# Kernel optimization log

Hardware: AMD Instinct MI355X
Metric: run time of the kernel (lower is better)

## Reference

```python
import jax, jax.numpy as jnp
import numpy as np

IN_DIM = 1024
OUT_DIM = 2048
GRID = 5   # kan_config.grid_size
K = 3      # kan_config.spline_order


def b_splines(x, grid, k):
    """Cox-de Boor recursion.
    x: (N, D), grid: (D, G+2k+1) extended knots. Returns (N, D, G+k) basis values."""
    x = x[..., None]              # (N, D, 1)
    g = grid[None, :, :]          # (1, D, M)
    # degree-0 indicator bases
    B = ((x >= g[..., :-1]) & (x < g[..., 1:])).astype(x.dtype)  # (N, D, M-1)
    for p in range(1, k + 1):
        left = (x - g[..., : -(p + 1)]) / (g[..., p:-1] - g[..., : -(p + 1)])
        right = (g[..., p + 1:] - x) / (g[..., p + 1:] - g[..., 1:-p])
        B = left * B[..., :-1] + right * B[..., 1:]
    return B  # (N, D, G+k)


def setup_inputs() -> dict:
    key = jax.random.key(0)
    k1, k2, k3 = jax.random.split(key, 3)
    # inputs kept inside the spline grid range [-1, 1]
    x = jax.random.uniform(k1, (4, 2048, IN_DIM), jnp.float32, -1.0, 1.0)
    # uniform extended grid over [-1, 1] with k extra knots on each side
    h = 2.0 / GRID
    g = jnp.arange(-K, GRID + K + 1, dtype=jnp.float32) * h - 1.0  # (G+2K+1,)
    grid = jnp.broadcast_to(g, (IN_DIM, GRID + 2 * K + 1)).astype(jnp.float32)
    coef = (jax.random.normal(k2, (IN_DIM, OUT_DIM, GRID + K), jnp.float32) * 0.1)
    scale_base = jax.random.normal(k3, (IN_DIM, OUT_DIM), jnp.float32) * 0.1 + (1.0 / np.sqrt(IN_DIM)).astype(np.float32)
    scale_sp = jnp.ones((IN_DIM, OUT_DIM), jnp.float32)
    return {"x": x, "grid": grid, "coef": coef, "scale_base": scale_base, "scale_sp": scale_sp}


def reference(x, grid, coef, scale_base, scale_sp):
    shp = x.shape
    xf = x.reshape(-1, shp[-1])                 # (N, D)
    B = b_splines(xf, grid, K)                  # (N, D, G+K)
    coef_s = coef * scale_sp[:, :, None]        # fold per-edge spline scale into coefficients
    spline = jnp.einsum('ndg,dog->no', B, coef_s)          # (N, O)
    base = jnp.einsum('nd,do->no', jax.nn.silu(xf), scale_base)  # (N, O)
    out = base + spline
    return out.reshape(shp[:-1] + (OUT_DIM,))
```

## Files before the change

### kernel.cpp

```cpp
#include <hip/hip_runtime.h>
#include <hip/hip_bf16.h>
#include <cstdint>

typedef unsigned short u16;
typedef __bf16 bf16x8 __attribute__((ext_vector_type(8)));
typedef float  f32x4  __attribute__((ext_vector_type(4)));

typedef const __attribute__((address_space(1))) void* gptr_t;
typedef __attribute__((address_space(3))) void*       sptr_t;

#define IN_DIM  1024
#define OUT_DIM 2048
#define NROWS   8192
#define NB      8
#define KTOT    (IN_DIM * 9)
#define KSPL    (IN_DIM * 8)

#define WT_O 16
#define WT_D 64
#define TR_BLOCKS ((NROWS / 64) * (IN_DIM / 64))
#define WT_BLOCKS ((OUT_DIM / WT_O) * (IN_DIM / WT_D))
#define ACT_BLOCKS ((NROWS / 64) * (IN_DIM / 64))

#define BK 32
#define TILE_U16 (256 * BK)
#define NKT (KTOT / BK)

__device__ __forceinline__ float rcp_fast(float v) { return __builtin_amdgcn_rcpf(v); }

__device__ __forceinline__ u16 f2b(float v) {
  uint32_t u = __float_as_uint(v);
  uint32_t r = (u + 0x7FFFu + ((u >> 16) & 1u)) >> 16;
  return (u16)r;
}

__device__ __forceinline__ uint32_t pkbf(float a, float b) {
  return (uint32_t)f2b(a) | ((uint32_t)f2b(b) << 16);
}

__device__ __forceinline__ uint4 basis_pack(float xval) {
  float tt = (xval + 1.0f) * 2.5f;
  float jf = floorf(tt);
  jf = fminf(fmaxf(jf, 0.0f), 4.0f);
  const float u = tt - jf;
  const int j = (int)jf;
  const float um = 1.0f - u;
  const float u2 = u * u, u3 = u2 * u;
  const float b0 = um * um * um * (1.0f / 6.0f);
  const float b1 = (3.0f * u3 - 6.0f * u2 + 4.0f) * (1.0f / 6.0f);
  const float b2 = (-3.0f * u3 + 3.0f * u2 + 3.0f * u + 1.0f) * (1.0f / 6.0f);
  const float b3 = u3 * (1.0f / 6.0f);
  const uint32_t e01 = pkbf(b0, b1), e23 = pkbf(b2, b3);
  const uint32_t o0 = e01 << 16;
  const uint32_t o12 = (e01 >> 16) | (e23 << 16);
  const uint32_t o3 = e23 >> 16;
  const int odd = j & 1, m = j >> 1;
  const uint32_t a0 = odd ? o0 : e01;
  const uint32_t a1 = odd ? o12 : e23;
  const uint32_t a2 = odd ? o3 : 0u;
  uint4 wv;
  wv.x = (m == 0) ? a0 : 0u;
  wv.y = (m == 1) ? a0 : ((m == 0) ? a1 : 0u);
  wv.z = (m == 2) ? a0 : ((m == 1) ? a1 : ((m == 0) ? a2 : 0u));
  wv.w = (m == 2) ? a1 : ((m == 1) ? a2 : 0u);
  return wv;
}

__global__ __launch_bounds__(256) void kan_prep2(const float* __restrict__ x,
                                                 const float* __restrict__ coef,
                                                 const float* __restrict__ scale_base,
                                                 const float* __restrict__ scale_sp,
                                                 u16* __restrict__ act,
                                                 u16* __restrict__ wt) {
  const int t = threadIdx.x;

  if (blockIdx.x < ACT_BLOCKS) {
    __shared__ __align__(16) u16 st[64][72];
    const int bi = blockIdx.x;
    const int n0 = (bi & 127) * 64;
    const int d0 = (bi >> 7) * 64;
    const int dl = t & 63, r0 = t >> 6;
#pragma unroll
    for (int i = 0; i < 16; ++i) {
      const int r = r0 + i * 4;
      const float v = x[(size_t)(n0 + r) * IN_DIM + d0 + dl];
      *(uint4*)&act[(size_t)(n0 + r) * KTOT + (size_t)(d0 + dl) * 8] = basis_pack(v);
      st[r][dl] = f2b(v * rcp_fast(1.0f + __expf(-v)));
    }
    __syncthreads();
#pragma unroll
    for (int j = 0; j < 2; ++j) {
      const int idx = t + j * 256;
      const int r = idx >> 3, c8 = idx & 7;
      *(uint4*)&act[(size_t)(n0 + r) * KTOT + KSPL + d0 + c8 * 8] =
          *(const uint4*)&st[r][c8 * 8];
    }
  } else {
    __shared__ __align__(16) u16 tsp[WT_O][WT_D * 8 + 8];
    __shared__ __align__(16) u16 tsi[WT_O][WT_D + 8];
    const int bi = blockIdx.x - ACT_BLOCKS;
    const int o0 = (bi % (OUT_DIM / WT_O)) * WT_O;
    const int d0 = (bi / (OUT_DIM / WT_O)) * WT_D;
    const int ol = t & (WT_O - 1), dl0 = t >> 4;
#pragma unroll
    for (int rep = 0; rep < WT_D / 16; ++rep) {
      const int dl = rep * 16 + dl0;
      const int d = d0 + dl, o = o0 + ol;
      const size_t doff = (size_t)d * OUT_DIM + o;
      const float ssp = scale_sp[doff];
      const float sbv = scale_base[doff];
      const float4* cp = (const float4*)(coef + doff * 8);
      float4 c0 = cp[0], c1 = cp[1];
      uint4 val;
      val.x = pkbf(c0.x * ssp, c0.y * ssp);
      val.y = pkbf(c0.z * ssp, c0.w * ssp);
      val.z = pkbf(c1.x * ssp, c1.y * ssp);
      val.w = pkbf(c1.z * ssp, c1.w * ssp);
      *(uint4*)&tsp[ol][dl * 8] = val;
      tsi[ol][dl] = f2b(sbv);
    }
    __syncthreads();
    for (int i = t; i < WT_O * 64; i += 256) {
      const int row = i >> 6, col = i & 63;
      *(uint4*)(wt + (size_t)(o0 + row) * KTOT + (size_t)(d0 + col) * 8) =
          *(const uint4*)&tsp[row][col * 8];
    }
    if (t < WT_O * 8) {
      const int row = t >> 3, col = t & 7;
      *(uint4*)(wt + (size_t)(o0 + row) * KTOT + KSPL + d0 + col * 8) =
          *(const uint4*)&tsi[row][col * 8];
    }
  }
}

__global__ __launch_bounds__(512, 2) void kan_gemm2(const u16* __restrict__ act,
                                                    const u16* __restrict__ Bt,
                                                    float* __restrict__ C) {
  __shared__ __align__(16) u16 As[4 * TILE_U16];
  __shared__ __align__(16) u16 Bs[4 * TILE_U16];
  const int tid  = threadIdx.x;
  const int lane = tid & 63;
  const int w    = tid >> 6;
  const int wm   = w >> 2, wn = w & 3;
  const int q    = lane >> 4, m16 = lane & 15;

  const int bid = (blockIdx.x & 7) * 32 + (blockIdx.x >> 3);
  const int gx = bid & 7;
  const int gy = bid >> 3;

  f32x4 acc[8][4];
#pragma unroll
  for (int i = 0; i < 8; ++i)
#pragma unroll
    for (int j = 0; j < 4; ++j) acc[i][j] = (f32x4){0.f, 0.f, 0.f, 0.f};

  const int rA  = lane >> 2;
  const int csw = ((lane & 3) ^ ((lane >> 3) & 3)) * 8;
  const u16* gA = act + (size_t)(gy * 256 + w * 32 + rA) * KTOT + csw;
  const u16* gB = Bt  + (size_t)(gx * 256 + w * 32 + rA) * KTOT + csw;
  const int ldsw = w * 1024;

#define STAGE(T)                                                               \
  do {                                                                         \
    const int _buf = (T) & 3;                                                  \
    const size_t _k0 = (size_t)(T) * BK;                                       \
    const u16* _ga = gA + _k0;                                                 \
    const u16* _gb = gB + _k0;                                                 \
    u16* _la = &As[_buf * TILE_U16 + ldsw];                                    \
    u16* _lb = &Bs[_buf * TILE_U16 + ldsw];                                    \
    __builtin_amdgcn_global_load_lds((gptr_t)_ga, (sptr_t)_la, 16, 0, 0);      \
    __builtin_amdgcn_global_load_lds((gptr_t)(_ga + (size_t)16 * KTOT),        \
                                     (sptr_t)(_la + 512), 16, 0, 0);           \
    __builtin_amdgcn_global_load_lds((gptr_t)_gb, (sptr_t)_lb, 16, 0, 0);      \
    __builtin_amdgcn_global_load_lds((gptr_t)(_gb + (size_t)16 * KTOT),        \
                                     (sptr_t)(_lb + 512), 16, 0, 0);           \
  } while (0)

  const int px8 = (q ^ ((m16 >> 1) & 3)) * 8;
  const int aoff = (wm * 128 + m16) * 32 + px8;
  const int boff = (wn * 64 + m16) * 32 + px8;

#define COMPUTE(T)                                                             \
  do {                                                                         \
    const int _buf = (T) & 3;                                                  \
    const u16* _A = &As[_buf * TILE_U16 + aoff];                               \
    const u16* _B = &Bs[_buf * TILE_U16 + boff];                               \
    bf16x8 _bf[4];                                                             \
    _Pragma("unroll") for (int nt = 0; nt < 4; ++nt)                           \
        _bf[nt] = *(const bf16x8*)&_B[nt * 512];                               \
    bf16x8 _af[8];                                                             \
    _Pragma("unroll") for (int mt = 0; mt < 8; ++mt)                           \
        _af[mt] = *(const bf16x8*)&_A[mt * 512];                               \
    __builtin_amdgcn_s_setprio(1);                                             \
    _Pragma("unroll") for (int mt = 0; mt < 8; ++mt)                           \
      _Pragma("unroll") for (int nt = 0; nt < 4; ++nt)                         \
          acc[mt][nt] = __builtin_amdgcn_mfma_f32_16x16x32_bf16(               \
              _af[mt], _bf[nt], acc[mt][nt], 0, 0, 0);                         \
    __builtin_amdgcn_s_setprio(0);                                             \
  } while (0)

#define KSTEP(T, VM, DOSTAGE)                                                  \
  do {                                                                         \
    if (DOSTAGE) STAGE((T) + 3);                                               \
    asm volatile("s_waitcnt vmcnt(" #VM ")" ::: "memory");                     \
    __builtin_amdgcn_s_barrier();                                              \
    COMPUTE(T);                                                                \
    asm volatile("" ::: "memory");                                             \
    __builtin_amdgcn_s_barrier();                                              \
  } while (0)

  STAGE(0);
  STAGE(1);
  STAGE(2);

  for (int tb = 0; tb < 71; ++tb) {
#pragma unroll
    for (int j = 0; j < 4; ++j) {
      const int t = tb * 4 + j;
      KSTEP(t, 12, true);
    }
  }
  KSTEP(284, 12, true);
  KSTEP(285, 8, false);
  KSTEP(286, 4, false);
  KSTEP(287, 0, false);

#undef KSTEP
#undef COMPUTE
#undef STAGE

  const int row_base = gy * 256 + wm * 128 + q * 4;
  const int col_base = gx * 256 + wn * 64 + m16;
#pragma unroll
  for (int mt = 0; mt < 8; ++mt) {
#pragma unroll
    for (int nt = 0; nt < 4; ++nt) {
      const int r0 = row_base + mt * 16;
      const int c  = col_base + nt * 16;
#pragma unroll
      for (int r = 0; r < 4; ++r)
        C[(size_t)(r0 + r) * OUT_DIM + c] = acc[mt][nt][r];
    }
  }
}

__global__ __launch_bounds__(256) void kan_prep(const float* __restrict__ x,
                                                const float* __restrict__ coef,
                                                const float* __restrict__ scale_base,
                                                const float* __restrict__ scale_sp,
                                                float* __restrict__ xT,
                                                u16* __restrict__ sil,
                                                u16* __restrict__ wt) {
  const int t = threadIdx.x;

  if (blockIdx.x < TR_BLOCKS) {
    __shared__ float tile[64][65];
    const int bi = blockIdx.x;
    const int n0 = (bi & 127) * 64;
    const int d0 = (bi >> 7) * 64;
    const int col = t & 63, rbase = t >> 6;
#pragma unroll
    for (int i = 0; i < 16; ++i) {
      const int r = rbase + i * 4;
      const float v = x[(size_t)(n0 + r) * IN_DIM + d0 + col];
      tile[r][col] = v;
      sil[(size_t)(n0 + r) * IN_DIM + d0 + col] =
          f2b(v * rcp_fast(1.0f + __expf(-v)));
    }
    __syncthreads();
#pragma unroll
    for (int i = 0; i < 16; ++i) {
      const int dd = rbase + i * 4;
      xT[(size_t)(d0 + dd) * NROWS + n0 + col] = tile[col][dd];
    }
  } else {
    __shared__ __align__(16) u16 tsp[WT_O][WT_D * 8 + 8];
    __shared__ __align__(16) u16 tsi[WT_O][WT_D + 8];
    const int bi = blockIdx.x - TR_BLOCKS;
    const int o0 = (bi % (OUT_DIM / WT_O)) * WT_O;
    const int d0 = (bi / (OUT_DIM / WT_O)) * WT_D;
    const int ol = t & (WT_O - 1), dl0 = t >> 4;
#pragma unroll
    for (int rep = 0; rep < WT_D / 16; ++rep) {
      const int dl = rep * 16 + dl0;
      const int d = d0 + dl, o = o0 + ol;
      const size_t doff = (size_t)d * OUT_DIM + o;
      const float ssp = scale_sp[doff];
      const float sbv = scale_base[doff];
      const float4* cp = (const float4*)(coef + doff * 8);
      float4 c0 = cp[0], c1 = cp[1];
      uint4 val;
      val.x = pkbf(c0.x * ssp, c0.y * ssp);
      val.y = pkbf(c0.z * ssp, c0.w * ssp);
      val.z = pkbf(c1.x * ssp, c1.y * ssp);
      val.w = pkbf(c1.z * ssp, c1.w * ssp);
      *(uint4*)&tsp[ol][dl * 8] = val;
      tsi[ol][dl] = f2b(sbv);
    }
    __syncthreads();
    for (int i = t; i < WT_O * 64; i += 256) {
      const int row = i >> 6, col = i & 63;
      *(uint4*)(wt + (size_t)(o0 + row) * KTOT + (size_t)(d0 + col) * 8) =
          *(const uint4*)&tsp[row][col * 8];
    }
    if (t < WT_O * 8) {
      const int row = t >> 3, col = t & 7;
      *(uint4*)(wt + (size_t)(o0 + row) * KTOT + KSPL + d0 + col * 8) =
          *(const uint4*)&tsi[row][col * 8];
    }
  }
}

__global__ __launch_bounds__(256) void kan_gemm(const float* __restrict__ xT,
                                                const u16* __restrict__ sil,
                                                const u16* __restrict__ Bt,
                                                float* __restrict__ C) {
  __shared__ __align__(16) u16 As[128 * 64];
  __shared__ __align__(16) u16 Bs[128 * 64];
  const int tid  = threadIdx.x;
  const int lane = tid & 63;
  const int w    = tid >> 6;
  const int wm   = w >> 1, wn = w & 1;
  const int q    = lane >> 4, m16 = lane & 15;
  const int gx = blockIdx.x, gy = blockIdx.y;

  f32x4 acc[4][4];
#pragma unroll
  for (int i = 0; i < 4; ++i)
#pragma unroll
    for (int j = 0; j < 4; ++j) acc[i][j] = (f32x4){0.f, 0.f, 0.f, 0.f};

  const int srow = lane >> 3;
  const int swzc = (lane & 7) ^ srow;
  const u16* gb0 = Bt + (size_t)(gx * 128) * KTOT + swzc * 8;
  const int r7 = m16 & 15 & 7;
  const int dgrp = tid >> 5;
  const int nh   = tid & 31;

  for (int kk = 0; kk < KTOT; kk += 64) {
#pragma unroll
    for (int i = 0; i < 4; ++i) {
      const int rg = w * 32 + i * 8;
      __builtin_amdgcn_global_load_lds((gptr_t)(gb0 + (size_t)(rg + srow) * KTOT + kk),
                                       (sptr_t)&Bs[rg * 64], 16, 0, 0);
    }
    if (kk < KSPL) {
      const int d = (kk >> 3) + dgrp;
      const float4 xv = *(const float4*)(xT + (size_t)d * NROWS + gy * 128 + nh * 4);
      const float xa[4] = {xv.x, xv.y, xv.z, xv.w};
#pragma unroll
      for (int r = 0; r < 4; ++r) {
        const int row = nh * 4 + r;
        const uint4 wv = basis_pack(xa[r]);
        *(uint4*)&As[row * 64 + ((dgrp ^ (row & 7)) * 8)] = wv;
      }
    } else {
      const int kb = kk - KSPL;
#pragma unroll
      for (int i = 0; i < 4; ++i) {
        const int rg = w * 32 + i * 8;
        __builtin_amdgcn_global_load_lds(
            (gptr_t)(sil + (size_t)(gy * 128 + rg + srow) * IN_DIM + kb + swzc * 8),
            (sptr_t)&As[rg * 64], 16, 0, 0);
      }
    }
    __syncthreads();
#pragma unroll
    for (int ks = 0; ks < 64; ks += 32) {
      const int pc = ((ks >> 3) + q) ^ r7;
      bf16x8 af[4], bf[4];
#pragma unroll
      for (int mt = 0; mt < 4; ++mt)
        af[mt] = *(const bf16x8*)&As[(wm * 64 + mt * 16 + m16) * 64 + pc * 8];
#pragma unroll
      for (int nt = 0; nt < 4; ++nt)
        bf[nt] = *(const bf16x8*)&Bs[(wn * 64 + nt * 16 + m16) * 64 + pc * 8];
#pragma unroll
      for (int mt = 0; mt < 4; ++mt)
#pragma unroll
        for (int nt = 0; nt < 4; ++nt)
          acc[mt][nt] = __builtin_amdgcn_mfma_f32_16x16x32_bf16(af[mt], bf[nt],
                                                                acc[mt][nt], 0, 0, 0);
    }
    __syncthreads();
  }

#pragma unroll
  for (int mt = 0; mt < 4; ++mt) {
    const int row0 = gy * 128 + wm * 64 + mt * 16 + q * 4;
#pragma unroll
    for (int nt = 0; nt < 4; ++nt) {
      const int col = gx * 128 + wn * 64 + nt * 16 + m16;
#pragma unroll
      for (int r = 0; r < 4; ++r)
        C[(size_t)(row0 + r) * OUT_DIM + col] = acc[mt][nt][r];
    }
  }
}

__global__ __launch_bounds__(256) void kan_fallback(const float* __restrict__ x,
                                                    const float* __restrict__ grid,
                                                    const float* __restrict__ coef,
                                                    const float* __restrict__ scale_base,
                                                    const float* __restrict__ scale_sp,
                                                    float* __restrict__ out) {
  __shared__ float bs[IN_DIM * 9];
  const int n = blockIdx.x;
  const int t = threadIdx.x;
#pragma unroll
  for (int dd = 0; dd < IN_DIM / 256; ++dd) {
    const int d = t + dd * 256;
    const float xv = x[(size_t)n * IN_DIM + d];
    float tt = (xv + 1.0f) * 2.5f;
    float jf = floorf(tt);
    jf = fminf(fmaxf(jf, 0.0f), 4.0f);
    const float u = tt - jf;
    const int j = (int)jf;
    const float um = 1.0f - u;
    const float u2 = u * u, u3 = u2 * u;
    float* r = &bs[d * 9];
#pragma unroll
    for (int g = 0; g < NB; ++g) r[g] = 0.0f;
    r[j]     = um * um * um * (1.0f / 6.0f);
    r[j + 1] = (3.0f * u3 - 6.0f * u2 + 4.0f) * (1.0f / 6.0f);
    r[j + 2] = (-3.0f * u3 + 3.0f * u2 + 3.0f * u + 1.0f) * (1.0f / 6.0f);
    r[j + 3] = u3 * (1.0f / 6.0f);
    r[8]     = xv * rcp_fast(1.0f + __expf(-xv));
  }
  __syncthreads();
  const int o = blockIdx.y * 256 + t;
  float acc = 0.0f;
  for (int d = 0; d < IN_DIM; ++d) {
    const size_t doff = (size_t)d * OUT_DIM + o;
    const float4* cp = (const float4*)(coef + doff * 8);
    float4 c0 = cp[0], c1 = cp[1];
    const float* b = &bs[d * 9];
    float s = b[0] * c0.x + b[1] * c0.y + b[2] * c0.z + b[3] * c0.w +
              b[4] * c1.x + b[5] * c1.y + b[6] * c1.z + b[7] * c1.w;
    acc += s * scale_sp[doff] + b[8] * scale_base[doff];
  }
  out[(size_t)n * OUT_DIM + o] = acc;
}

extern "C" void kernel_launch(void* const* d_in, const int* in_sizes, int n_in,
                              void* d_out, int out_size, void* d_ws, size_t ws_size,
                              hipStream_t stream) {
  const float* x  = (const float*)d_in[0];
  const float* gr = (const float*)d_in[1];
  const float* cf = (const float*)d_in[2];
  const float* sb = (const float*)d_in[3];
  const float* sp = (const float*)d_in[4];
  float* out = (float*)d_out;

  const size_t act_bytes = (size_t)NROWS * KTOT * sizeof(u16);
  const size_t wt_bytes  = (size_t)OUT_DIM * KTOT * sizeof(u16);
  const size_t need1 = act_bytes + wt_bytes;

  const size_t xT_bytes  = (size_t)IN_DIM * NROWS * sizeof(float);
  const size_t sil_bytes = (size_t)NROWS * IN_DIM * sizeof(u16);
  const size_t need2 = xT_bytes + sil_bytes + wt_bytes;

  if (ws_size >= need1) {
    u16* act = (u16*)d_ws;
    u16* wt  = (u16*)((char*)d_ws + act_bytes);
    kan_prep2<<<dim3(ACT_BLOCKS + WT_BLOCKS), dim3(256), 0, stream>>>(
        x, cf, sb, sp, act, wt);
    kan_gemm2<<<dim3(256), dim3(512), 0, stream>>>(act, wt, out);
  } else if (ws_size >= need2) {
    float* xT = (float*)d_ws;
    u16* sil  = (u16*)((char*)d_ws + xT_bytes);
    u16* wt   = (u16*)((char*)d_ws + xT_bytes + sil_bytes);
    kan_prep<<<dim3(TR_BLOCKS + WT_BLOCKS), dim3(256), 0, stream>>>(
        x, cf, sb, sp, xT, sil, wt);
    kan_gemm<<<dim3(OUT_DIM / 128, NROWS / 128), dim3(256), 0, stream>>>(
        xT, sil, wt, out);
  } else {
    kan_fallback<<<dim3(NROWS, OUT_DIM / 256), dim3(256), 0, stream>>>(x, gr, cf, sb, sp, out);
  }
}
```

Measured before the change: 474.8 us.

## Software-pipeline LDS fragment reads behind MFMAs with one barrier per k-step

```diff
diff --git a/kernel.cpp b/kernel.cpp
--- a/kernel.cpp
+++ b/kernel.cpp
@@ -180,53 +180,64 @@
   const int aoff = (wm * 128 + m16) * 32 + px8;
   const int boff = (wn * 64 + m16) * 32 + px8;
 
-#define COMPUTE(T)                                                             \
+  bf16x8 fa[8], fb[4];
+
+#define REGION(T, DOREAD, DOSTAGE, VM)                                         \
   do {                                                                         \
-    const int _buf = (T) & 3;                                                  \
-    const u16* _A = &As[_buf * TILE_U16 + aoff];                               \
-    const u16* _B = &Bs[_buf * TILE_U16 + boff];                               \
-    bf16x8 _bf[4];                                                             \
-    _Pragma("unroll") for (int nt = 0; nt < 4; ++nt)                           \
-        _bf[nt] = *(const bf16x8*)&_B[nt * 512];                               \
-    bf16x8 _af[8];                                                             \
-    _Pragma("unroll") for (int mt = 0; mt < 8; ++mt)                           \
-        _af[mt] = *(const bf16x8*)&_A[mt * 512];                               \
+    const u16* _An = &As[(((T) + 1) & 3) * TILE_U16 + aoff];                   \
+    const u16* _Bn = &Bs[(((T) + 1) & 3) * TILE_U16 + boff];                   \
+    if (DOSTAGE) STAGE((T) + 4);                                               \
     __builtin_amdgcn_s_setprio(1);                                             \
-    _Pragma("unroll") for (int mt = 0; mt < 8; ++mt)                           \
+    _Pragma("unroll") for (int mt = 0; mt < 8; ++mt) {                         \
       _Pragma("unroll") for (int nt = 0; nt < 4; ++nt)                         \
-          acc[mt][nt] = __builtin_amdgcn_mfma_f32_16x16x32_bf16(               \
-              _af[mt], _bf[nt], acc[mt][nt], 0, 0, 0);                         \
+        acc[mt][nt] = __builtin_amdgcn_mfma_f32_16x16x32_bf16(                 \
+            fa[mt], fb[nt], acc[mt][nt], 0, 0, 0);                             \
+      if (DOREAD) fa[mt] = *(const bf16x8*)&_An[mt * 512];                     \
+    }                                                                          \
     __builtin_amdgcn_s_setprio(0);                                             \
-  } while (0)
-
-#define KSTEP(T, VM, DOSTAGE)                                                  \
-  do {                                                                         \
-    if (DOSTAGE) STAGE((T) + 3);                                               \
+    if (DOREAD) {                                                              \
+      _Pragma("unroll") for (int nt = 0; nt < 4; ++nt)                         \
+        fb[nt] = *(const bf16x8*)&_Bn[nt * 512];                               \
+    }                                                                          \
     asm volatile("s_waitcnt vmcnt(" #VM ")" ::: "memory");                     \
-    __builtin_amdgcn_s_barrier();                                              \
-    COMPUTE(T);                                                                \
-    asm volatile("" ::: "memory");                                             \
+    asm volatile("s_waitcnt lgkmcnt(0)" ::: "memory");                         \
     __builtin_amdgcn_s_barrier();                                              \
   } while (0)
 
   STAGE(0);
   STAGE(1);
   STAGE(2);
+  STAGE(3);
+  asm volatile("s_waitcnt vmcnt(8)" ::: "memory");
+  __builtin_amdgcn_s_barrier();
+  {
+    const u16* _A0 = &As[aoff];
+    const u16* _B0 = &Bs[boff];
+#pragma unroll
+    for (int nt = 0; nt < 4; ++nt) fb[nt] = *(const bf16x8*)&_B0[nt * 512];
+#pragma unroll
+    for (int mt = 0; mt < 8; ++mt) fa[mt] = *(const bf16x8*)&_A0[mt * 512];
+  }
 
   for (int tb = 0; tb < 71; ++tb) {
 #pragma unroll
     for (int j = 0; j < 4; ++j) {
-      const int t = tb * 4 + j;
-      KSTEP(t, 12, true);
-    }
-  }
-  KSTEP(284, 12, true);
-  KSTEP(285, 8, false);
-  KSTEP(286, 4, false);
-  KSTEP(287, 0, false);
-
-#undef KSTEP
-#undef COMPUTE
+      REGION(tb * 4 + j, true, true, 8);
+    }
+  }
+  REGION(284, true, false, 4);
+  REGION(285, true, false, 0);
+  REGION(286, true, false, 0);
+  __builtin_amdgcn_s_setprio(1);
+#pragma unroll
+  for (int mt = 0; mt < 8; ++mt)
+#pragma unroll
+    for (int nt = 0; nt < 4; ++nt)
+      acc[mt][nt] = __builtin_amdgcn_mfma_f32_16x16x32_bf16(fa[mt], fb[nt],
+                                                            acc[mt][nt], 0, 0, 0);
+  __builtin_amdgcn_s_setprio(0);
+
+#undef REGION
 #undef STAGE
 
   const int row_base = gy * 256 + wm * 128 + q * 4;
```

New measurement: 443.9 us. 6.5% less time.

## Split GEMM k-step into two half-tile phases to overlap LDS reads with MFMA

Applied to the files above, without the earlier changes.

```diff
diff --git a/kernel.cpp b/kernel.cpp
--- a/kernel.cpp
+++ b/kernel.cpp
@@ -180,53 +180,76 @@
   const int aoff = (wm * 128 + m16) * 32 + px8;
   const int boff = (wn * 64 + m16) * 32 + px8;
 
-#define COMPUTE(T)                                                             \
+  bf16x8 fa[4], fb[4];
+
+#define PHASE_A(T, DOSTAGE)                                                    \
   do {                                                                         \
-    const int _buf = (T) & 3;                                                  \
-    const u16* _A = &As[_buf * TILE_U16 + aoff];                               \
-    const u16* _B = &Bs[_buf * TILE_U16 + boff];                               \
-    bf16x8 _bf[4];                                                             \
-    _Pragma("unroll") for (int nt = 0; nt < 4; ++nt)                           \
-        _bf[nt] = *(const bf16x8*)&_B[nt * 512];                               \
-    bf16x8 _af[8];                                                             \
-    _Pragma("unroll") for (int mt = 0; mt < 8; ++mt)                           \
-        _af[mt] = *(const bf16x8*)&_A[mt * 512];                               \
+    const u16* _Ab = &As[((T) & 3) * TILE_U16 + aoff];                         \
+    const u16* _Bb = &Bs[((T) & 3) * TILE_U16 + boff];                         \
+    _Pragma("unroll") for (int i = 0; i < 4; ++i)                              \
+        fa[i] = *(const bf16x8*)&_Ab[i * 512];                                 \
+    _Pragma("unroll") for (int i = 0; i < 4; ++i)                              \
+        fb[i] = *(const bf16x8*)&_Bb[i * 512];                                 \
+    if (DOSTAGE) STAGE((T) + 3);                                               \
+    asm volatile("" ::: "memory");                                             \
+    __builtin_amdgcn_s_barrier();                                              \
+    asm volatile("s_waitcnt lgkmcnt(0)" ::: "memory");                         \
     __builtin_amdgcn_s_setprio(1);                                             \
-    _Pragma("unroll") for (int mt = 0; mt < 8; ++mt)                           \
+    _Pragma("unroll") for (int mt = 0; mt < 4; ++mt)                           \
       _Pragma("unroll") for (int nt = 0; nt < 4; ++nt)                         \
-          acc[mt][nt] = __builtin_amdgcn_mfma_f32_16x16x32_bf16(               \
-              _af[mt], _bf[nt], acc[mt][nt], 0, 0, 0);                         \
+        acc[mt][nt] = __builtin_amdgcn_mfma_f32_16x16x32_bf16(                 \
+            fa[mt], fb[nt], acc[mt][nt], 0, 0, 0);                             \
     __builtin_amdgcn_s_setprio(0);                                             \
+    asm volatile("" ::: "memory");                                             \
+    __builtin_amdgcn_s_barrier();                                              \
+    asm volatile("" ::: "memory");                                             \
   } while (0)
 
-#define KSTEP(T, VM, DOSTAGE)                                                  \
+#define PHASE_B(T, VM)                                                         \
   do {                                                                         \
-    if (DOSTAGE) STAGE((T) + 3);                                               \
+    const u16* _Ab = &As[((T) & 3) * TILE_U16 + aoff + 2048];                  \
+    _Pragma("unroll") for (int i = 0; i < 4; ++i)                              \
+        fa[i] = *(const bf16x8*)&_Ab[i * 512];                                 \
     asm volatile("s_waitcnt vmcnt(" #VM ")" ::: "memory");                     \
     __builtin_amdgcn_s_barrier();                                              \
-    COMPUTE(T);                                                                \
+    asm volatile("s_waitcnt lgkmcnt(0)" ::: "memory");                         \
+    __builtin_amdgcn_s_setprio(1);                                             \
+    _Pragma("unroll") for (int mt = 0; mt < 4; ++mt)                           \
+      _Pragma("unroll") for (int nt = 0; nt < 4; ++nt)                         \
+        acc[4 + mt][nt] = __builtin_amdgcn_mfma_f32_16x16x32_bf16(             \
+            fa[mt], fb[nt], acc[4 + mt][nt], 0, 0, 0);                         \
+    __builtin_amdgcn_s_setprio(0);                                             \
     asm volatile("" ::: "memory");                                             \
     __builtin_amdgcn_s_barrier();                                              \
+    asm volatile("" ::: "memory");                                             \
   } while (0)
 
   STAGE(0);
   STAGE(1);
   STAGE(2);
+  asm volatile("s_waitcnt vmcnt(8)" ::: "memory");
+  __builtin_amdgcn_s_barrier();
+  asm volatile("" ::: "memory");
 
   for (int tb = 0; tb < 71; ++tb) {
 #pragma unroll
     for (int j = 0; j < 4; ++j) {
       const int t = tb * 4 + j;
-      KSTEP(t, 12, true);
-    }
-  }
-  KSTEP(284, 12, true);
-  KSTEP(285, 8, false);
-  KSTEP(286, 4, false);
-  KSTEP(287, 0, false);
-
-#undef KSTEP
-#undef COMPUTE
+      PHASE_A(t, true);
+      PHASE_B(t, 8);
+    }
+  }
+  PHASE_A(284, true);
+  PHASE_B(284, 8);
+  PHASE_A(285, false);
+  PHASE_B(285, 4);
+  PHASE_A(286, false);
+  PHASE_B(286, 0);
+  PHASE_A(287, false);
+  PHASE_B(287, 0);
+
+#undef PHASE_A
+#undef PHASE_B
 #undef STAGE
 
   const int row_base = gy * 256 + wm * 128 + q * 4;
```

New measurement: 507.6 us. 1.07x slower.
